# Kernel optimization log

Measured on AMD Instinct MI355X. Metric: run time of the kernel, lower is better.

Reference implementation:

```python
import jax, jax.numpy as jnp
import numpy as np

B, N, C_IN, C_COORD, K = 2, 8192, 64, 3, 16
C_CAT = C_IN + C_COORD  # 67
HID1, HID2, C_OUT = 32, 64, 64


def setup_inputs() -> dict:
    key = jax.random.key(0)
    ks = jax.random.split(key, 10)
    s = 0.05
    return {
        "point_features": jax.random.normal(ks[0], (B, N, C_IN), jnp.float32),
        "coords": jax.random.uniform(ks[1], (B, N, C_COORD), jnp.float32),
        "w1": jax.random.normal(ks[2], (HID1, C_CAT), jnp.float32) * s,
        "b1": jax.random.normal(ks[3], (HID1,), jnp.float32) * s,
        "w2": jax.random.normal(ks[4], (HID2, HID1), jnp.float32) * s,
        "b2": jax.random.normal(ks[5], (HID2,), jnp.float32) * s,
        "w3": jax.random.normal(ks[6], (C_OUT, HID2), jnp.float32) * s,
        "b3": jax.random.normal(ks[7], (C_OUT,), jnp.float32) * s,
        "aggr_w": jax.random.normal(ks[8], (K,), jnp.float32) * s,
        "aggr_b": jax.random.normal(ks[9], (1,), jnp.float32) * s,
    }


def _knn_idx(coords):
    # squared pairwise distances: [B, N, N]
    sq = jnp.sum(coords * coords, axis=-1)
    d2 = sq[:, :, None] + sq[:, None, :] - 2.0 * jnp.einsum("bnc,bmc->bnm", coords, coords)
    # k smallest distances -> top_k of negated; self (d=0) lands at slot 0
    _, idx = jax.lax.top_k(-d2, K)  # [B, N, K]
    return idx


def reference(point_features, coords, w1, b1, w2, b2, w3, b3, aggr_w, aggr_b):
    idx = _knn_idx(coords)  # [B, N, K] int32
    feats = jnp.concatenate([point_features, coords], axis=-1)  # [B, N, C_CAT]
    # gather neighbor features -> [B, N, K, C_CAT]
    g = jax.vmap(lambda f, i: f[i])(feats, idx)
    # relative coords w.r.t. neighbor 0 (self)
    rel = g[..., -C_COORD:] - g[:, :, 0:1, -C_COORD:]
    g = jnp.concatenate([g[..., :C_IN], rel], axis=-1)
    # point pooling: max over K of raw input-feature channels
    y_pool = jnp.max(g[..., :C_IN], axis=2)  # [B, N, C_IN]
    # kernel MLP: stacked 1x1 convs, NO activations (act_func=None in source)
    h = jnp.einsum("bnkc,oc->bnko", g, w1) + b1
    h = jnp.einsum("bnkc,oc->bnko", h, w2) + b2
    h = jnp.einsum("bnkc,oc->bnko", h, w3) + b3  # [B, N, K, C_OUT]
    # attentive aggregation: Conv2d(K, 1, 1) over the K axis
    y_aggr = jnp.einsum("bnko,k->bno", h, aggr_w) + aggr_b  # [B, N, C_OUT]
    out_sum = jnp.sum(h, axis=2)  # [B, N, C_OUT]
    # concat order matches torch: (sum, pool, aggr), then permute -> B x N x C'
    return jnp.concatenate([out_sum, y_pool, y_aggr], axis=-1)
```

## Files before the change

### kernel.cpp

```cpp
#include <hip/hip_runtime.h>
#include <stdint.h>


typedef unsigned short u16;
typedef unsigned int   u32;
typedef unsigned long long u64;

#define NPTS  8192
#define KNB   16
#define SCAP  128

__device__ __forceinline__ float bf2f(u16 u) {
    union { u32 i; float f; } v; v.i = ((u32)u) << 16; return v.f;
}
__device__ __forceinline__ u16 f2bf(float f) {
    u32 x = __float_as_uint(f);
    return (u16)((x + 0x7FFFu + ((x >> 16) & 1u)) >> 16);
}
__device__ __forceinline__ u32 fordkey(float f) {
    u32 u = __float_as_uint(f);
    return u ^ ((u32)((int)u >> 31) | 0x80000000u);
}
__device__ __forceinline__ u64 shflxor64(u64 v, int m) {
    int lo = __shfl_xor((int)(u32)v, m, 64);
    int hi = __shfl_xor((int)(u32)(v >> 32), m, 64);
    return ((u64)(u32)hi << 32) | (u32)lo;
}
__device__ __forceinline__ float sq_np32(float x, float y, float z) {
    return __fadd_rn(__fadd_rn(__fmul_rn(x, x), __fmul_rn(y, y)), __fmul_rn(z, z));
}
__device__ __forceinline__ float d2_ref(float qx, float qy, float qz, float qsq,
                                        float x, float y, float z, float sq) {
    float dot = fmaf(z, qz, fmaf(y, qy, __fmul_rn(x, qx)));
    return __fsub_rn(__fadd_rn(qsq, sq), __fmul_rn(2.0f, dot));
}
__device__ __forceinline__ int cellof(float v) {
    int c = (int)floorf(v * 8.0f);
    return c < 0 ? 0 : (c > 7 ? 7 : c);
}

__global__ __launch_bounds__(256) void pack_count_kernel(
    const float* __restrict__ pf, const float* __restrict__ coords,
    u16* __restrict__ pfh, int* __restrict__ counts) {
    int gid = blockIdx.x * 256 + threadIdx.x;
    pfh[gid] = f2bf(pf[gid]);
    if (gid < 2 * NPTS) {
        float x = coords[gid * 3 + 0];
        float y = coords[gid * 3 + 1];
        float z = coords[gid * 3 + 2];
        int b = gid >> 13;
        int cell = (cellof(x) * 8 + cellof(y)) * 8 + cellof(z);
        atomicAdd(&counts[b * 512 + cell], 1);
    }
}

__global__ __launch_bounds__(512) void scan_kernel(
    const int* __restrict__ counts, int* __restrict__ cellStart,
    int* __restrict__ cellOffset) {
    __shared__ int s[512];
    int b = blockIdx.x, t = threadIdx.x;
    int myc = counts[b * 512 + t];
    s[t] = myc; __syncthreads();
#pragma unroll
    for (int o = 1; o < 512; o <<= 1) {
        int v = (t >= o) ? s[t - o] : 0; __syncthreads();
        s[t] += v; __syncthreads();
    }
    int excl = s[t] - myc;
    cellStart[b * 513 + t] = excl;
    cellOffset[b * 512 + t] = excl;
    if (t == 511) cellStart[b * 513 + 512] = s[511];
}

__global__ __launch_bounds__(256) void scatter_kernel(
    const float* __restrict__ coords, int* __restrict__ cellOffset,
    float4* __restrict__ spts, int* __restrict__ sidx) {
    int gid = blockIdx.x * 256 + threadIdx.x;
    float x = coords[gid * 3 + 0];
    float y = coords[gid * 3 + 1];
    float z = coords[gid * 3 + 2];
    int b = gid >> 13, i = gid & (NPTS - 1);
    int cell = (cellof(x) * 8 + cellof(y)) * 8 + cellof(z);
    int pos = atomicAdd(&cellOffset[b * 512 + cell], 1);
    spts[b * NPTS + pos] = make_float4(x, y, z, sq_np32(x, y, z));
    sidx[b * NPTS + pos] = i;
}

__global__ __launch_bounds__(256) void prep_kernel(
    const float* __restrict__ w1, const float* __restrict__ b1,
    const float* __restrict__ w2, const float* __restrict__ b2,
    const float* __restrict__ w3, const float* __restrict__ b3,
    float* __restrict__ M, float* __restrict__ E) {
    __shared__ float W1s[32 * 67];
    __shared__ float W2s[64 * 32];
    __shared__ float W3s[64 * 64];
    __shared__ float T[64][68];
    __shared__ float tb2[64];
    int t = threadIdx.x;
    for (int i = t; i < 32 * 67; i += 256) W1s[i] = w1[i];
    for (int i = t; i < 64 * 32; i += 256) W2s[i] = w2[i];
    for (int i = t; i < 64 * 64; i += 256) W3s[i] = w3[i];
    __syncthreads();
#pragma unroll 1
    for (int e = t; e < 64 * 67; e += 256) {
        int row = e / 67, c = e - row * 67;
        float acc = 0.0f;
#pragma unroll
        for (int i = 0; i < 32; ++i)
            acc = fmaf(W2s[row * 32 + i], W1s[i * 67 + c], acc);
        T[row][c] = acc;
    }
    if (t < 64) {
        float accb = 0.0f;
#pragma unroll
        for (int i = 0; i < 32; ++i) accb = fmaf(W2s[t * 32 + i], b1[i], accb);
        tb2[t] = accb + b2[t];
        T[t][67] = 0.0f;
    }
    __syncthreads();
#pragma unroll 1
    for (int e = t; e < 64 * 67; e += 256) {
        int row = e / 67, c = e - row * 67;
        float acc = 0.0f;
#pragma unroll
        for (int j = 0; j < 64; ++j)
            acc = fmaf(W3s[row * 64 + j], T[j][c], acc);
        M[row * 68 + c] = acc;
    }
    if (t < 64) {
        M[t * 68 + 67] = 0.0f;
        float e2 = 0.0f;
#pragma unroll
        for (int j = 0; j < 64; ++j) e2 = fmaf(W3s[t * 64 + j], tb2[j], e2);
        E[t] = e2 + b3[t];
    }
}

__global__ __launch_bounds__(128) void knnmlp_kernel(
    const float* __restrict__ coords, const float4* __restrict__ spts,
    const int* __restrict__ sidx, const int* __restrict__ cellStart,
    const u16* __restrict__ pfh, const float* __restrict__ M,
    const float* __restrict__ E, const float* __restrict__ aw,
    const float* __restrict__ ab, float* __restrict__ out) {

    __shared__ u64 surv[2][SCAP];
    __shared__ __attribute__((aligned(16))) float vb[2][2][68];

    const int lane = threadIdx.x & 63;
    const int wv   = threadIdx.x >> 6;
    const int sblk = ((int)blockIdx.x & 7) * 1024 + ((int)blockIdx.x >> 3);
    const int pos  = sblk * 2 + wv;
    const int b    = pos >> 13;
    const int p    = pos & (NPTS - 1);
    const float*  cb = coords + (size_t)b * NPTS * 3;
    const float4* sp = spts + b * NPTS;
    const int*    si = sidx + b * NPTS;
    const int*    cs = cellStart + b * 513;
    u64* sv = surv[wv];

    const int q = si[p];
    float qx = cb[q * 3 + 0], qy = cb[q * 3 + 1], qz = cb[q * 3 + 2];
    float qsq = sq_np32(qx, qy, qz);
    int cqx = cellof(qx), cqy = cellof(qy), cqz = cellof(qz);

    int ax0 = max(cqx - 1, 0), ax1 = min(cqx + 1, 7);
    int ay0 = max(cqy - 1, 0), ay1 = min(cqy + 1, 7);
    int az0 = max(cqz - 1, 0), az1 = min(cqz + 1, 7);
    float dmin = 3.0e38f;
#pragma unroll 1
    for (int cx = ax0; cx <= ax1; ++cx)
#pragma unroll 1
        for (int cy = ay0; cy <= ay1; ++cy) {
            int base = (cx * 8 + cy) * 8;
            int s = cs[base + az0], e = cs[base + az1 + 1];
            for (int i0 = s; i0 < e; i0 += 64) {
                int i = i0 + lane;
                int ii = (i < e) ? i : (e - 1);
                float4 c = sp[ii];
                float d2 = d2_ref(qx, qy, qz, qsq, c.x, c.y, c.z, c.w);
                if (i < e) dmin = fminf(dmin, d2);
            }
        }
    {
        float v = dmin;
#pragma unroll
        for (int k = 2; k <= 64; k <<= 1) {
#pragma unroll
            for (int j2 = k >> 1; j2 >= 1; j2 >>= 1) {
                float o = __shfl_xor(v, j2, 64);
                bool lo = (lane & j2) == 0;
                bool up = (lane & k) == 0;
                float mn = fminf(v, o), mx = fmaxf(v, o);
                v = (lo == up) ? mn : mx;
            }
        }
        dmin = __shfl(v, 15, 64);
    }
    const float tau = dmin;

    float rr = sqrtf(tau + 1e-5f) + 1e-6f;
    int bx0 = max((int)floorf((qx - rr) * 8.0f), 0);
    int bx1 = min((int)floorf((qx + rr) * 8.0f), 7);
    int by0 = max((int)floorf((qy - rr) * 8.0f), 0);
    int by1 = min((int)floorf((qy + rr) * 8.0f), 7);
    int bz0 = max((int)floorf((qz - rr) * 8.0f), 0);
    int bz1 = min((int)floorf((qz + rr) * 8.0f), 7);
    int cnt = 0;
#pragma unroll 1
    for (int cx = bx0; cx <= bx1; ++cx)
#pragma unroll 1
        for (int cy = by0; cy <= by1; ++cy) {
            int base = (cx * 8 + cy) * 8;
            int s = cs[base + bz0], e = cs[base + bz1 + 1];
            for (int i0 = s; i0 < e; i0 += 64) {
                int i = i0 + lane;
                bool valid = (i < e);
                int ii = valid ? i : (e - 1);
                float4 c = sp[ii];
                float d2 = d2_ref(qx, qy, qz, qsq, c.x, c.y, c.z, c.w);
                bool pass = valid && (d2 <= tau);
                u64 mask = __ballot(pass);
                if (pass) {
                    int pre = __builtin_amdgcn_mbcnt_hi((u32)(mask >> 32),
                              __builtin_amdgcn_mbcnt_lo((u32)mask, 0));
                    int pp = cnt + pre;
                    if (pp < SCAP)
                        sv[pp] = ((u64)fordkey(d2) << 32) | (u32)si[ii];
                }
                cnt += (int)__popcll(mask);
            }
        }
    __threadfence_block();

    int myidx = 0;
    if (cnt <= 64) {
        u64 key = (lane < cnt) ? sv[lane] : ~0ull;
#pragma unroll
        for (int k = 2; k <= 64; k <<= 1) {
#pragma unroll
            for (int j2 = k >> 1; j2 >= 1; j2 >>= 1) {
                u64 o = shflxor64(key, j2);
                bool lo = (lane & j2) == 0;
                bool up = (lane & k) == 0;
                bool takemin = (lo == up);
                key = ((o < key) == takemin) ? o : key;
            }
        }
        myidx = (int)(u32)(key & 0xffffffffu);
    } else {
        int cc = cnt > SCAP ? SCAP : cnt;
        u64 a0 = (lane < cc) ? sv[lane] : ~0ull;
        u64 a1 = (64 + lane < cc) ? sv[64 + lane] : ~0ull;
        if (a1 < a0) { u64 tmp = a0; a0 = a1; a1 = tmp; }
#pragma unroll 1
        for (int r2 = 0; r2 < 16; ++r2) {
            u64 mm = a0;
#pragma unroll
            for (int d = 1; d < 64; d <<= 1) {
                u64 o = shflxor64(mm, d);
                mm = (o < mm) ? o : mm;
            }
            if (a0 == mm) { a0 = a1; a1 = ~0ull; }
            if (lane == r2) myidx = (int)(u32)(mm & 0xffffffffu);
        }
    }

    __builtin_amdgcn_sched_barrier(0);

    float awr[16];
#pragma unroll
    for (int k = 0; k < 16; ++k) awr[k] = aw[k];
    float sa = 0.0f;
#pragma unroll
    for (int k = 0; k < 16; ++k) sa += awr[k];
    const float ev = E[lane], abv = ab[0];
    const u16* pfb = pfh + (size_t)b * NPTS * 64;

    float pool = -3.0e38f, G1 = 0.0f, Ga = 0.0f;
#pragma unroll
    for (int k = 0; k < 16; ++k) {
        int nk = __shfl(myidx, k, 64);
        float v = bf2f(pfb[nk * 64 + lane]);
        pool = fmaxf(pool, v);
        G1 += v;
        Ga = fmaf(awr[k], v, Ga);
    }
    float* v0 = vb[wv][0];
    float* v1 = vb[wv][1];
    v0[lane] = G1;
    v1[lane] = Ga;
    if (lane < 48) {
        int j1 = lane >> 4;
        int nk2 = __shfl(myidx, lane & 15, 64);
        int i0  = __shfl(myidx, 0, 64);
        float rel  = cb[nk2 * 3 + j1] - cb[i0 * 3 + j1];
        float wrel = awr[lane & 15] * rel;
#pragma unroll
        for (int d = 1; d < 16; d <<= 1) {
            rel  += __shfl_xor(rel, d, 64);
            wrel += __shfl_xor(wrel, d, 64);
        }
        if ((lane & 15) == 0) { v0[64 + j1] = rel; v1[64 + j1] = wrel; }
    }
    if (lane == 0) { v0[67] = 0.0f; v1[67] = 0.0f; }
    __threadfence_block();

    float s1 = 16.0f * ev, sA = sa * ev;
    {
        const float4* mp = (const float4*)(M + lane * 68);
        const float4* p0 = (const float4*)v0;
        const float4* p1 = (const float4*)v1;
#pragma unroll
        for (int c4 = 0; c4 < 17; ++c4) {
            float4 mr = mp[c4];
            float4 x0 = p0[c4], x1 = p1[c4];
            s1 = fmaf(x0.x, mr.x, s1); s1 = fmaf(x0.y, mr.y, s1);
            s1 = fmaf(x0.z, mr.z, s1); s1 = fmaf(x0.w, mr.w, s1);
            sA = fmaf(x1.x, mr.x, sA); sA = fmaf(x1.y, mr.y, sA);
            sA = fmaf(x1.z, mr.z, sA); sA = fmaf(x1.w, mr.w, sA);
        }
    }
    float* op = out + ((size_t)b * NPTS + q) * 192;
    op[lane]       = s1;
    op[64 + lane]  = pool;
    op[128 + lane] = sA + abv;
}

extern "C" void kernel_launch(void* const* d_in, const int* in_sizes, int n_in,
                              void* d_out, int out_size, void* d_ws, size_t ws_size,
                              hipStream_t stream) {
    const float* pf     = (const float*)d_in[0];
    const float* coords = (const float*)d_in[1];
    const float* w1     = (const float*)d_in[2];
    const float* b1     = (const float*)d_in[3];
    const float* w2     = (const float*)d_in[4];
    const float* b2     = (const float*)d_in[5];
    const float* w3     = (const float*)d_in[6];
    const float* b3     = (const float*)d_in[7];
    const float* aw     = (const float*)d_in[8];
    const float* ab     = (const float*)d_in[9];

    char* ws = (char*)d_ws;
    u16*    pfh        = (u16*)ws;
    float4* spts       = (float4*)(ws + (2 << 20));
    int*    sidx       = (int*)(ws + (2 << 20) + (256 << 10));
    int*    cellStart  = (int*)(ws + (2 << 20) + (320 << 10));
    int*    counts     = (int*)(ws + (2 << 20) + (328 << 10));
    int*    cellOffset = (int*)(ws + (2 << 20) + (336 << 10));
    float*  Mw         = (float*)(ws + (2 << 20) + (344 << 10));
    float*  Ew         = (float*)(ws + (2 << 20) + (364 << 10));
    float*  outp       = (float*)d_out;

    hipMemsetAsync(counts, 0, 2 * 512 * sizeof(int), stream);
    pack_count_kernel<<<4096, 256, 0, stream>>>(pf, coords, pfh, counts);
    scan_kernel<<<2, 512, 0, stream>>>(counts, cellStart, cellOffset);
    scatter_kernel<<<64, 256, 0, stream>>>(coords, cellOffset, spts, sidx);
    prep_kernel<<<1, 256, 0, stream>>>(w1, b1, w2, b2, w3, b3, Mw, Ew);
    knnmlp_kernel<<<8192, 128, 0, stream>>>(coords, spts, sidx, cellStart, pfh,
                                            Mw, Ew, aw, ab, outp);
}
```

Measured before the change: 155.4 us.

## Fuse grid-build preprocessing kernels into one cooperative kernel with grid syncs

Merges the memset, bf16 pack/count, scan, scatter and weight-folding kernels into a single cooperative launch of 128 blocks, separated by grid.sync barriers. The goal is to remove several kernel launches and inter-kernel gaps ahead of the main kNN/MLP kernel. The bf16 pack now uses float4 loads and ushort4 stores, and the scan becomes a single-wave shuffle scan. The cost is grid-wide barrier latency, plus the weight folding running on one block alongside the pack work.

```diff
diff --git a/kernel.cpp b/kernel.cpp
--- a/kernel.cpp
+++ b/kernel.cpp
@@ -1,6 +1,9 @@
 #include <hip/hip_runtime.h>
+#include <hip/hip_cooperative_groups.h>
 #include <stdint.h>
 
+
+namespace cg = cooperative_groups;
 
 typedef unsigned short u16;
 typedef unsigned int   u32;
@@ -39,12 +42,81 @@
     return c < 0 ? 0 : (c > 7 ? 7 : c);
 }
 
-__global__ __launch_bounds__(256) void pack_count_kernel(
+__global__ __launch_bounds__(256) void build_kernel(
     const float* __restrict__ pf, const float* __restrict__ coords,
-    u16* __restrict__ pfh, int* __restrict__ counts) {
-    int gid = blockIdx.x * 256 + threadIdx.x;
-    pfh[gid] = f2bf(pf[gid]);
-    if (gid < 2 * NPTS) {
+    const float* __restrict__ w1, const float* __restrict__ b1,
+    const float* __restrict__ w2, const float* __restrict__ b2,
+    const float* __restrict__ w3, const float* __restrict__ b3,
+    u16* __restrict__ pfh, int* __restrict__ counts,
+    int* __restrict__ cellStart, int* __restrict__ cellOffset,
+    float4* __restrict__ spts, int* __restrict__ sidx,
+    float* __restrict__ M, float* __restrict__ E) {
+
+    cg::grid_group grid = cg::this_grid();
+    const int blk = blockIdx.x;
+    const int tid = threadIdx.x;
+
+    if (blk < 4) counts[blk * 256 + tid] = 0;
+    {
+        const float4* pf4 = (const float4*)pf;
+        ushort4* ph4 = (ushort4*)pfh;
+#pragma unroll
+        for (int i = 0; i < 8; ++i) {
+            int g = (blk * 256 + tid) * 8 + i;
+            float4 v = pf4[g];
+            ushort4 o;
+            o.x = f2bf(v.x); o.y = f2bf(v.y); o.z = f2bf(v.z); o.w = f2bf(v.w);
+            ph4[g] = o;
+        }
+    }
+    if (blk == 127) {
+        __shared__ float W1s[32 * 67];
+        __shared__ float W2s[64 * 32];
+        __shared__ float W3s[64 * 64];
+        __shared__ float T[64][68];
+        __shared__ float tb2[64];
+        for (int i = tid; i < 32 * 67; i += 256) W1s[i] = w1[i];
+        for (int i = tid; i < 64 * 32; i += 256) W2s[i] = w2[i];
+        for (int i = tid; i < 64 * 64; i += 256) W3s[i] = w3[i];
+        __syncthreads();
+#pragma unroll 1
+        for (int e = tid; e < 64 * 67; e += 256) {
+            int row = e / 67, c = e - row * 67;
+            float acc = 0.0f;
+#pragma unroll
+            for (int i = 0; i < 32; ++i)
+                acc = fmaf(W2s[row * 32 + i], W1s[i * 67 + c], acc);
+            T[row][c] = acc;
+        }
+        if (tid < 64) {
+            float accb = 0.0f;
+#pragma unroll
+            for (int i = 0; i < 32; ++i) accb = fmaf(W2s[tid * 32 + i], b1[i], accb);
+            tb2[tid] = accb + b2[tid];
+            T[tid][67] = 0.0f;
+        }
+        __syncthreads();
+#pragma unroll 1
+        for (int e = tid; e < 64 * 67; e += 256) {
+            int row = e / 67, c = e - row * 67;
+            float acc = 0.0f;
+#pragma unroll
+            for (int j = 0; j < 64; ++j)
+                acc = fmaf(W3s[row * 64 + j], T[j][c], acc);
+            M[row * 68 + c] = acc;
+        }
+        if (tid < 64) {
+            M[tid * 68 + 67] = 0.0f;
+            float e2 = 0.0f;
+#pragma unroll
+            for (int j = 0; j < 64; ++j) e2 = fmaf(W3s[tid * 64 + j], tb2[j], e2);
+            E[tid] = e2 + b3[tid];
+        }
+    }
+    grid.sync();
+
+    if (tid < 128) {
+        int gid = blk * 128 + tid;
         float x = coords[gid * 3 + 0];
         float y = coords[gid * 3 + 1];
         float z = coords[gid * 3 + 2];
@@ -52,87 +124,40 @@
         int cell = (cellof(x) * 8 + cellof(y)) * 8 + cellof(z);
         atomicAdd(&counts[b * 512 + cell], 1);
     }
-}
-
-__global__ __launch_bounds__(512) void scan_kernel(
-    const int* __restrict__ counts, int* __restrict__ cellStart,
-    int* __restrict__ cellOffset) {
-    __shared__ int s[512];
-    int b = blockIdx.x, t = threadIdx.x;
-    int myc = counts[b * 512 + t];
-    s[t] = myc; __syncthreads();
-#pragma unroll
-    for (int o = 1; o < 512; o <<= 1) {
-        int v = (t >= o) ? s[t - o] : 0; __syncthreads();
-        s[t] += v; __syncthreads();
-    }
-    int excl = s[t] - myc;
-    cellStart[b * 513 + t] = excl;
-    cellOffset[b * 512 + t] = excl;
-    if (t == 511) cellStart[b * 513 + 512] = s[511];
-}
-
-__global__ __launch_bounds__(256) void scatter_kernel(
-    const float* __restrict__ coords, int* __restrict__ cellOffset,
-    float4* __restrict__ spts, int* __restrict__ sidx) {
-    int gid = blockIdx.x * 256 + threadIdx.x;
-    float x = coords[gid * 3 + 0];
-    float y = coords[gid * 3 + 1];
-    float z = coords[gid * 3 + 2];
-    int b = gid >> 13, i = gid & (NPTS - 1);
-    int cell = (cellof(x) * 8 + cellof(y)) * 8 + cellof(z);
-    int pos = atomicAdd(&cellOffset[b * 512 + cell], 1);
-    spts[b * NPTS + pos] = make_float4(x, y, z, sq_np32(x, y, z));
-    sidx[b * NPTS + pos] = i;
-}
-
-__global__ __launch_bounds__(256) void prep_kernel(
-    const float* __restrict__ w1, const float* __restrict__ b1,
-    const float* __restrict__ w2, const float* __restrict__ b2,
-    const float* __restrict__ w3, const float* __restrict__ b3,
-    float* __restrict__ M, float* __restrict__ E) {
-    __shared__ float W1s[32 * 67];
-    __shared__ float W2s[64 * 32];
-    __shared__ float W3s[64 * 64];
-    __shared__ float T[64][68];
-    __shared__ float tb2[64];
-    int t = threadIdx.x;
-    for (int i = t; i < 32 * 67; i += 256) W1s[i] = w1[i];
-    for (int i = t; i < 64 * 32; i += 256) W2s[i] = w2[i];
-    for (int i = t; i < 64 * 64; i += 256) W3s[i] = w3[i];
-    __syncthreads();
-#pragma unroll 1
-    for (int e = t; e < 64 * 67; e += 256) {
-        int row = e / 67, c = e - row * 67;
-        float acc = 0.0f;
-#pragma unroll
-        for (int i = 0; i < 32; ++i)
-            acc = fmaf(W2s[row * 32 + i], W1s[i * 67 + c], acc);
-        T[row][c] = acc;
-    }
-    if (t < 64) {
-        float accb = 0.0f;
-#pragma unroll
-        for (int i = 0; i < 32; ++i) accb = fmaf(W2s[t * 32 + i], b1[i], accb);
-        tb2[t] = accb + b2[t];
-        T[t][67] = 0.0f;
-    }
-    __syncthreads();
-#pragma unroll 1
-    for (int e = t; e < 64 * 67; e += 256) {
-        int row = e / 67, c = e - row * 67;
-        float acc = 0.0f;
-#pragma unroll
-        for (int j = 0; j < 64; ++j)
-            acc = fmaf(W3s[row * 64 + j], T[j][c], acc);
-        M[row * 68 + c] = acc;
-    }
-    if (t < 64) {
-        M[t * 68 + 67] = 0.0f;
-        float e2 = 0.0f;
-#pragma unroll
-        for (int j = 0; j < 64; ++j) e2 = fmaf(W3s[t * 64 + j], tb2[j], e2);
-        E[t] = e2 + b3[t];
+    grid.sync();
+
+    if (blk < 2 && tid < 64) {
+        const int lane = tid;
+        int running = 0;
+#pragma unroll 1
+        for (int c = 0; c < 8; ++c) {
+            int idx = blk * 512 + c * 64 + lane;
+            int val = counts[idx];
+            int incl = val;
+#pragma unroll
+            for (int d = 1; d < 64; d <<= 1) {
+                int o = __shfl_up(incl, d, 64);
+                if (lane >= d) incl += o;
+            }
+            int excl = running + incl - val;
+            cellStart[blk * 513 + c * 64 + lane] = excl;
+            cellOffset[blk * 512 + c * 64 + lane] = excl;
+            running += __shfl(incl, 63, 64);
+        }
+        if (lane == 0) cellStart[blk * 513 + 512] = running;
+    }
+    grid.sync();
+
+    if (tid < 128) {
+        int gid = blk * 128 + tid;
+        float x = coords[gid * 3 + 0];
+        float y = coords[gid * 3 + 1];
+        float z = coords[gid * 3 + 2];
+        int b = gid >> 13, i = gid & (NPTS - 1);
+        int cell = (cellof(x) * 8 + cellof(y)) * 8 + cellof(z);
+        int pos = atomicAdd(&cellOffset[b * 512 + cell], 1);
+        spts[b * NPTS + pos] = make_float4(x, y, z, sq_np32(x, y, z));
+        sidx[b * NPTS + pos] = i;
     }
 }
 
@@ -351,11 +376,14 @@
     float*  Ew         = (float*)(ws + (2 << 20) + (364 << 10));
     float*  outp       = (float*)d_out;
 
-    hipMemsetAsync(counts, 0, 2 * 512 * sizeof(int), stream);
-    pack_count_kernel<<<4096, 256, 0, stream>>>(pf, coords, pfh, counts);
-    scan_kernel<<<2, 512, 0, stream>>>(counts, cellStart, cellOffset);
-    scatter_kernel<<<64, 256, 0, stream>>>(coords, cellOffset, spts, sidx);
-    prep_kernel<<<1, 256, 0, stream>>>(w1, b1, w2, b2, w3, b3, Mw, Ew);
+    void* argsB[] = {
+        (void*)&pf, (void*)&coords, (void*)&w1, (void*)&b1, (void*)&w2,
+        (void*)&b2, (void*)&w3, (void*)&b3, (void*)&pfh, (void*)&counts,
+        (void*)&cellStart, (void*)&cellOffset, (void*)&spts, (void*)&sidx,
+        (void*)&Mw, (void*)&Ew
+    };
+    hipLaunchCooperativeKernel((const void*)build_kernel, dim3(128), dim3(256),
+                               argsB, 0, stream);
     knnmlp_kernel<<<8192, 128, 0, stream>>>(coords, spts, sidx, cellStart, pfh,
                                             Mw, Ew, aw, ab, outp);
 }
```

Measured after the change: 219.3 us. 41.1% more time.
